# Optimization experiments

Hardware: AMD Instinct MI355X
Metric: run time of the kernel (lower is better)

The kernel has to match this reference:

```python
import jax, jax.numpy as jnp
import numpy as np

EPS = 1e-12

def l2norm(x):
    # torch F.normalize(p=2, dim=-1): x / max(||x||, eps)
    n = jnp.sqrt(jnp.sum(x * x, axis=-1, keepdims=True))
    return x / jnp.maximum(n, EPS)

def grid_sample_zeros(img, grid):
    """Bilinear grid_sample, padding_mode='zeros', align_corners=False.
    img: [B,C,H,W], grid: [B,P,2] with (x,y) in [-1,1]. Returns [B,C,P]."""
    B, C, H, W = img.shape
    ix = ((grid[..., 0] + 1.0) * W - 1.0) * 0.5  # [B,P]
    iy = ((grid[..., 1] + 1.0) * H - 1.0) * 0.5
    x0 = jnp.floor(ix); x1 = x0 + 1.0
    y0 = jnp.floor(iy); y1 = y0 + 1.0
    wx1 = ix - x0; wx0 = 1.0 - wx1
    wy1 = iy - y0; wy0 = 1.0 - wy1

    def gather(xf, yf):
        valid = ((xf >= 0) & (xf <= W - 1) & (yf >= 0) & (yf <= H - 1)).astype(img.dtype)
        xi = jnp.clip(xf, 0, W - 1).astype(jnp.int32)
        yi = jnp.clip(yf, 0, H - 1).astype(jnp.int32)
        v = jax.vmap(lambda im, yy, xx: im[:, yy, xx])(img, yi, xi)  # [B,C,P]
        return v * valid[:, None, :]

    out = (gather(x0, y0) * (wx0 * wy0)[:, None, :]
         + gather(x1, y0) * (wx1 * wy0)[:, None, :]
         + gather(x0, y1) * (wx0 * wy1)[:, None, :]
         + gather(x1, y1) * (wx1 * wy1)[:, None, :])
    return out


def setup_inputs() -> dict:
    key = jax.random.key(0)
    ks = jax.random.split(key, 8)
    B, N, K, C = 4, 512, 128, 256
    H8 = W8 = 128
    H16 = W16 = 64
    inp = {
        'node_reliability_weights': jax.random.normal(ks[0], (B, N), jnp.float32),
        'node_features': jax.random.normal(ks[1], (B, N, C), jnp.float32),
        'rel_map_8': jax.random.normal(ks[2], (B, H8, W8), jnp.float32),
        'feat_map_8': jax.random.normal(ks[3], (B, C, H8, W8), jnp.float32),
        'rel_map_16': jax.random.normal(ks[4], (B, H16, W16), jnp.float32),
        'feat_map_16': jax.random.normal(ks[5], (B, C, H16, W16), jnp.float32),
        # normalized coords in [-1,1]
        'coords': jax.random.uniform(ks[6], (B, K, N, 2), jnp.float32) * 2.0 - 1.0,
        'logit_scale': jnp.asarray(np.log(1.0 / 0.07), jnp.float32),
    }
    return inp


def reference(node_reliability_weights, node_features, rel_map_8, feat_map_8,
              rel_map_16, feat_map_16, coords, logit_scale):
    B, N, C = node_features.shape
    K = coords.shape[1]
    nnf = l2norm(node_features)  # [B,N,C]
    # [B,K,N,2] -> [B,N,K,2] -> [B,N*K,2]
    grid = jnp.transpose(coords, (0, 2, 1, 3)).reshape(B, N * K, 2)

    sims, rels = [], []
    for rel_map, feat_map in ((rel_map_8, feat_map_8), (rel_map_16, feat_map_16)):
        sr = grid_sample_zeros(rel_map[:, None], grid).reshape(B, N, K)
        sf = grid_sample_zeros(feat_map, grid).reshape(B, C, N, K)
        nsf = l2norm(jnp.transpose(sf, (0, 2, 3, 1)))  # [B,N,K,C]
        sims.append(jnp.einsum('bnc,bnkc->bnk', nnf, nsf))
        rels.append(node_reliability_weights[:, :, None] + sr)

    S = len(sims)
    total_sim = jnp.stack(sims, axis=-1)  # [B,N,K,S]
    total_rel = jnp.stack(rels, axis=-1)  # [B,N,K,S]
    total_rel = jnp.transpose(total_rel, (0, 2, 1, 3)).reshape(B, K, N * S)
    total_rel = jax.nn.softmax(total_rel, axis=-1)
    total_sim = jnp.transpose(total_sim, (0, 2, 1, 3)).reshape(B, K, N * S)
    logits = jnp.sum(total_sim * total_rel, axis=-1) * jnp.exp(logit_scale)  # [B,K]
    return jax.nn.softmax(logits, axis=1)
```

## Files before the change

kernel.cpp:

```cpp
#include <hip/hip_runtime.h>
#include <math.h>

typedef _Float16 f16;
typedef _Float16 f16x2 __attribute__((ext_vector_type(2)));
typedef _Float16 f16x4 __attribute__((ext_vector_type(4)));

namespace {
constexpr int B = 4, N = 512, K = 128, C = 256;
constexpr int H8 = 128, W8 = 128, P8 = H8 * W8;
constexpr int H16 = 64, W16 = 64, P16 = H16 * W16;
constexpr int NBG = 32;
constexpr int LBINS = NBG * NBG;
constexpr int NBINS = B * LBINS;
constexpr int NSAMP = B * K * N;
constexpr int WROW = 528;
constexpr int TBX = P8 / 64 + P16 / 64;
constexpr int NCB = NSAMP / 512 / 16;
}

__device__ __forceinline__ float fdot2a(f16x2 a, f16x2 b, float c)
{
#if __has_builtin(__builtin_amdgcn_fdot2)
    return __builtin_amdgcn_fdot2(a, b, c, false);
#else
    return c + (float)a.x * (float)b.x + (float)a.y * (float)b.y;
#endif
}

__device__ __forceinline__ float red16_sum(float x)
{
    int t;
    t = __builtin_amdgcn_update_dpp(0, __float_as_int(x), 0xB1,  0xF, 0xF, true);
    x += __int_as_float(t);
    t = __builtin_amdgcn_update_dpp(0, __float_as_int(x), 0x4E,  0xF, 0xF, true);
    x += __int_as_float(t);
    t = __builtin_amdgcn_update_dpp(0, __float_as_int(x), 0x141, 0xF, 0xF, true);
    x += __int_as_float(t);
    t = __builtin_amdgcn_update_dpp(0, __float_as_int(x), 0x140, 0xF, 0xF, true);
    x += __int_as_float(t);
    return x;
}

__device__ __forceinline__ int band32(float g)
{
    int v = (int)((g + 1.0f) * 0.5f * NBG);
    return min(NBG - 1, max(0, v));
}

__device__ __forceinline__ void blend_dot(
    const float4* A, const float4* Bv, const float* w, const f16x2* nf,
    float& dot, float& n2)
{
    f16x2 v[8];
    {
        const f16 h = (f16)w[0];
        const f16x2 w0{h, h};
        const f16x2* a0 = reinterpret_cast<const f16x2*>(&A[0]);
        const f16x2* b0 = reinterpret_cast<const f16x2*>(&Bv[0]);
#pragma unroll
        for (int c = 0; c < 4; ++c) { v[c] = w0 * a0[c]; v[c + 4] = w0 * b0[c]; }
    }
#pragma unroll
    for (int t = 1; t < 4; ++t) {
        const f16 h = (f16)w[t];
        const f16x2 wt{h, h};
        const f16x2* at = reinterpret_cast<const f16x2*>(&A[t]);
        const f16x2* bt = reinterpret_cast<const f16x2*>(&Bv[t]);
#pragma unroll
        for (int c = 0; c < 4; ++c) { v[c] += wt * at[c]; v[c + 4] += wt * bt[c]; }
    }
    float d0 = 0, d1 = 0, m0 = 0, m1 = 0;
#pragma unroll
    for (int c = 0; c < 4; ++c) { d0 = fdot2a(nf[c], v[c], d0); m0 = fdot2a(v[c], v[c], m0); }
#pragma unroll
    for (int c = 4; c < 8; ++c) { d1 = fdot2a(nf[c], v[c], d1); m1 = fdot2a(v[c], v[c], m1); }
    dot = red16_sum(d0 + d1);
    n2  = red16_sum(m0 + m1);
}

__global__ __launch_bounds__(256) void k_prep(
    const float* __restrict__ in8, const float* __restrict__ in16,
    f16* __restrict__ o8, f16* __restrict__ o16,
    const float* __restrict__ coords, unsigned* __restrict__ hist)
{
    __shared__ float tile[64][65];
    const int tid = threadIdx.x;
    int bx = blockIdx.x;

    if (bx >= TBX) {
        unsigned* cnt = reinterpret_cast<unsigned*>(tile);
        const int cblk = (bx - TBX) * 16 + blockIdx.y * 4 + blockIdx.z;
        const int sid0 = cblk * 512;
        const int b = sid0 >> 16;
        for (int i = tid; i < LBINS; i += 256) cnt[i] = 0;
        __syncthreads();
#pragma unroll
        for (int j = 0; j < 2; ++j) {
            const int sid = sid0 + j * 256 + tid;
            const float gx = coords[(size_t)sid * 2 + 0];
            const float gy = coords[(size_t)sid * 2 + 1];
            atomicAdd(&cnt[band32(gy) * NBG + band32(gx)], 1u);
        }
        __syncthreads();
        for (int i = tid; i < LBINS; i += 256)
            if (cnt[i]) atomicAdd(&hist[b * LBINS + i], cnt[i]);
        return;
    }

    const float* in; f16* out; int P;
    if (bx < P8 / 64) { in = in8; out = o8; P = P8; }
    else { bx -= P8 / 64; in = in16; out = o16; P = P16; }
    const int b  = blockIdx.z;
    const int p0 = bx * 64;
    const int c0 = blockIdx.y * 64;
    const int tp = tid & 63, tq = tid >> 6;
    const float* src = in + (size_t)b * C * P;
    f16* dst = out + (size_t)b * P * C;
#pragma unroll
    for (int i = 0; i < 16; ++i) {
        const int cl = tq + i * 4;
        tile[cl][tp] = src[(size_t)(c0 + cl) * P + (p0 + tp)];
    }
    __syncthreads();
#pragma unroll
    for (int i = 0; i < 16; ++i) {
        const int pl = tq + i * 4;
        dst[(size_t)(p0 + pl) * C + (c0 + tp)] = (f16)tile[tp][pl];
    }
}

__global__ __launch_bounds__(256) void k_scan(
    const unsigned* __restrict__ hist, unsigned* __restrict__ cursor,
    unsigned* __restrict__ binofs)
{
    __shared__ unsigned sums[256];
    const int t = threadIdx.x;
    unsigned v[16];
    unsigned s = 0;
#pragma unroll
    for (int i = 0; i < 16; ++i) { v[i] = s; s += hist[t * 16 + i]; }
    sums[t] = s;
    __syncthreads();
    for (int off = 1; off < 256; off <<= 1) {
        const unsigned x = (t >= off) ? sums[t - off] : 0u;
        __syncthreads();
        sums[t] += x;
        __syncthreads();
    }
    const unsigned pre = (t == 0) ? 0u : sums[t - 1];
#pragma unroll
    for (int i = 0; i < 16; ++i) {
        cursor[t * 16 + i] = pre + v[i];
        binofs[t * 16 + i] = pre + v[i];
    }
    if (t == 255) binofs[NBINS] = sums[255];
}

__global__ __launch_bounds__(256) void k_scatprep(
    const float* __restrict__ coords, unsigned* __restrict__ cursor,
    unsigned* __restrict__ order,
    const float* __restrict__ nodef, f16* __restrict__ nnf)
{
    const int tid = threadIdx.x;
    if (blockIdx.x >= NSAMP / 512) {
        const int node = (blockIdx.x - NSAMP / 512) * 4 + (tid >> 6);
        const int lane = tid & 63;
        const float4 v = *reinterpret_cast<const float4*>(
            nodef + (size_t)node * C + lane * 4);
        float nn = v.x * v.x + v.y * v.y + v.z * v.z + v.w * v.w;
#pragma unroll
        for (int off = 32; off; off >>= 1) nn += __shfl_xor(nn, off);
        const float inv = __frsqrt_rn(fmaxf(nn, 1e-24f));
        f16x4 o;
        o.x = (f16)(v.x * inv); o.y = (f16)(v.y * inv);
        o.z = (f16)(v.z * inv); o.w = (f16)(v.w * inv);
        *reinterpret_cast<f16x4*>(nnf + (size_t)node * C + lane * 4) = o;
        return;
    }

    __shared__ unsigned cnt[LBINS], base[LBINS];
    const int sid0 = blockIdx.x * 512;
    const int b = sid0 >> 16;
    for (int i = tid; i < LBINS; i += 256) cnt[i] = 0;
    __syncthreads();
    int bl[2];
#pragma unroll
    for (int j = 0; j < 2; ++j) {
        const int sid = sid0 + j * 256 + tid;
        const float gx = coords[(size_t)sid * 2 + 0];
        const float gy = coords[(size_t)sid * 2 + 1];
        bl[j] = band32(gy) * NBG + band32(gx);
        atomicAdd(&cnt[bl[j]], 1u);
    }
    __syncthreads();
    for (int i = tid; i < LBINS; i += 256)
        base[i] = cnt[i] ? atomicAdd(&cursor[b * LBINS + i], cnt[i]) : 0u;
    __syncthreads();
    for (int i = tid; i < LBINS; i += 256) cnt[i] = 0;
    __syncthreads();
#pragma unroll
    for (int j = 0; j < 2; ++j) {
        const int sid = sid0 + j * 256 + tid;
        const unsigned r = base[bl[j]] + atomicAdd(&cnt[bl[j]], 1u);
        order[r] = (unsigned)sid;
    }
}

__global__ __launch_bounds__(256) void k_sample(
    const float* __restrict__ nodew,
    const f16*  __restrict__ nnf,
    const float* __restrict__ rel8,
    const float* __restrict__ rel16,
    const float* __restrict__ coords,
    const f16*  __restrict__ ft8,
    const f16*  __restrict__ ft16,
    const unsigned* __restrict__ order,
    const unsigned* __restrict__ binofs,
    float4* __restrict__ sr)
{
    const int bin = ((blockIdx.x & 7) * (NBINS / 8)) + (blockIdx.x >> 3);
    const int b = bin >> 10, lb = bin & (LBINS - 1);
    const int by = lb >> 5, bx = lb & 31;
    const int tid = threadIdx.x;
    const int grp = tid >> 4, gl = tid & 15;
    const int y0w = 4 * by - 1, x0w = 4 * bx - 1;
    const int y0q = 2 * by - 1, x0q = 2 * bx - 1;

    const unsigned s0 = binofs[bin];
    const int cnt = (int)(binofs[bin + 1] - s0);
    if (cnt == 0) return;

    __shared__ __align__(16) unsigned char lds[36 * WROW];
    __shared__ float srel8[36], srel16[16];

    const f16* f8b = ft8 + (size_t)b * P8 * C;
    const f16* fqb = ft16 + (size_t)b * P16 * C;
    const float* r8b = rel8 + (size_t)b * P8;
    const float* rqb = rel16 + (size_t)b * P16;

    for (int i = tid; i < 36 * 33; i += 256) {
        const int r = i / 33, c = i - r * 33;
        const int wy = r / 6, wx = r - wy * 6;
        const int py = min(max(y0w + wy, 0), H8 - 1);
        const int px = min(max(x0w + wx, 0), W8 - 1);
        uint4 v{0, 0, 0, 0};
        if (c < 32)
            v = *reinterpret_cast<const uint4*>(
                f8b + ((size_t)(py * W8 + px)) * C + c * 8);
        *reinterpret_cast<uint4*>(&lds[r * WROW + c * 16]) = v;
    }
    if (tid < 36) {
        const int wy = tid / 6, wx = tid - wy * 6;
        const int py = min(max(y0w + wy, 0), H8 - 1);
        const int px = min(max(x0w + wx, 0), W8 - 1);
        srel8[tid] = r8b[py * W8 + px];
    } else if (tid < 52) {
        const int i = tid - 36;
        const int wy = i >> 2, wx = i & 3;
        const int py = min(max(y0q + wy, 0), H16 - 1);
        const int px = min(max(x0q + wx, 0), W16 - 1);
        srel16[i] = rqb[py * W16 + px];
    }
    __syncthreads();

    for (int basei = 0; basei < cnt; basei += 16) {
        const int idx = basei + grp;
        const bool active = idx < cnt;
        const unsigned sid = order[s0 + (active ? idx : 0)];
        const int n = sid & 511, k = (sid >> 9) & 127;
        const float gx = coords[(size_t)sid * 2 + 0];
        const float gy = coords[(size_t)sid * 2 + 1];

        const f16* np_ = nnf + (size_t)(b * N + n) * C;
        const float4 nr0 = *reinterpret_cast<const float4*>(np_ + gl * 8);
        const float4 nr1 = *reinterpret_cast<const float4*>(np_ + 128 + gl * 8);
        f16x2 nf[8];
        {
            const f16x2* h0 = reinterpret_cast<const f16x2*>(&nr0);
            const f16x2* h1 = reinterpret_cast<const f16x2*>(&nr1);
#pragma unroll
            for (int c = 0; c < 4; ++c) { nf[c] = h0[c]; nf[c + 4] = h1[c]; }
        }

        float wq[4]; int qx0, qx1, qy0, qy1;
        {
            const float ix = ((gx + 1.f) * W16 - 1.f) * 0.5f;
            const float iy = ((gy + 1.f) * H16 - 1.f) * 0.5f;
            const float x0f = floorf(ix), y0f = floorf(iy);
            const int x0 = (int)x0f, y0 = (int)y0f, x1 = x0 + 1, y1 = y0 + 1;
            const float fx1 = ix - x0f, fx0 = 1.f - fx1;
            const float fy1 = iy - y0f, fy0 = 1.f - fy1;
            const bool vx0 = x0 >= 0 && x0 < W16, vx1 = x1 >= 0 && x1 < W16;
            const bool vy0 = y0 >= 0 && y0 < H16, vy1 = y1 >= 0 && y1 < H16;
            wq[0] = vx0 && vy0 ? fx0 * fy0 : 0.f;
            wq[1] = vx1 && vy0 ? fx1 * fy0 : 0.f;
            wq[2] = vx0 && vy1 ? fx0 * fy1 : 0.f;
            wq[3] = vx1 && vy1 ? fx1 * fy1 : 0.f;
            qx0 = min(max(x0, 0), W16 - 1); qx1 = min(max(x1, 0), W16 - 1);
            qy0 = min(max(y0, 0), H16 - 1); qy1 = min(max(y1, 0), H16 - 1);
        }
        const int qp[4] = {qy0 * W16 + qx0, qy0 * W16 + qx1,
                           qy1 * W16 + qx0, qy1 * W16 + qx1};
        float4 ga[4], gb[4];
#pragma unroll
        for (int t = 0; t < 4; ++t) {
            const f16* tp = fqb + (size_t)qp[t] * C;
            ga[t] = *reinterpret_cast<const float4*>(tp + gl * 8);
            gb[t] = *reinterpret_cast<const float4*>(tp + 128 + gl * 8);
        }

        float wp[4]; int sx0, sx1, sy0, sy1;
        {
            const float ix = ((gx + 1.f) * W8 - 1.f) * 0.5f;
            const float iy = ((gy + 1.f) * H8 - 1.f) * 0.5f;
            const float x0f = floorf(ix), y0f = floorf(iy);
            const int x0 = (int)x0f, y0 = (int)y0f, x1 = x0 + 1, y1 = y0 + 1;
            const float fx1 = ix - x0f, fx0 = 1.f - fx1;
            const float fy1 = iy - y0f, fy0 = 1.f - fy1;
            const bool vx0 = x0 >= 0 && x0 < W8, vx1 = x1 >= 0 && x1 < W8;
            const bool vy0 = y0 >= 0 && y0 < H8, vy1 = y1 >= 0 && y1 < H8;
            wp[0] = vx0 && vy0 ? fx0 * fy0 : 0.f;
            wp[1] = vx1 && vy0 ? fx1 * fy0 : 0.f;
            wp[2] = vx0 && vy1 ? fx0 * fy1 : 0.f;
            wp[3] = vx1 && vy1 ? fx1 * fy1 : 0.f;
            sx0 = min(max(x0, 0), W8 - 1); sx1 = min(max(x1, 0), W8 - 1);
            sy0 = min(max(y0, 0), H8 - 1); sy1 = min(max(y1, 0), H8 - 1);
        }
        const int wxa = min(max(sx0 - x0w, 0), 5), wxb = min(max(sx1 - x0w, 0), 5);
        const int wya = min(max(sy0 - y0w, 0), 5), wyb = min(max(sy1 - y0w, 0), 5);
        const int lr[4] = {wya * 6 + wxa, wya * 6 + wxb,
                           wyb * 6 + wxa, wyb * 6 + wxb};
        float4 la[4], lbv[4];
#pragma unroll
        for (int t = 0; t < 4; ++t) {
            la[t]  = *reinterpret_cast<const float4*>(&lds[lr[t] * WROW + gl * 16]);
            lbv[t] = *reinterpret_cast<const float4*>(&lds[lr[t] * WROW + 256 + gl * 16]);
        }

        float dot8, n28;
        blend_dot(la, lbv, wp, nf, dot8, n28);
        const float sim8 = dot8 * __frsqrt_rn(fmaxf(n28, 1e-24f));
        const float rv8 = wp[0] * srel8[lr[0]] + wp[1] * srel8[lr[1]]
                        + wp[2] * srel8[lr[2]] + wp[3] * srel8[lr[3]];

        float dotq, n2q;
        blend_dot(ga, gb, wq, nf, dotq, n2q);
        const float simq = dotq * __frsqrt_rn(fmaxf(n2q, 1e-24f));
        const int qwxa = min(max(qx0 - x0q, 0), 3), qwxb = min(max(qx1 - x0q, 0), 3);
        const int qwya = min(max(qy0 - y0q, 0), 3), qwyb = min(max(qy1 - y0q, 0), 3);
        const float rvq = wq[0] * srel16[qwya * 4 + qwxa] + wq[1] * srel16[qwya * 4 + qwxb]
                        + wq[2] * srel16[qwyb * 4 + qwxa] + wq[3] * srel16[qwyb * 4 + qwxb];

        if (active && gl == 0) {
            const float wr = nodew[b * N + n];
            sr[(size_t)(b * K + k) * N + n] =
                make_float4(sim8, simq, wr + rv8, wr + rvq);
        }
    }
}

__global__ __launch_bounds__(256) void k_logits(
    const float4* __restrict__ sr, const float* __restrict__ lscale,
    float* __restrict__ logits)
{
    const int bk = blockIdx.x;
    const int tid = threadIdx.x;
    const int lane = tid & 63, wid = tid >> 6;
    const float4* sp = sr + (size_t)bk * N;
    __shared__ float red0[4], red1[4], red2[4];

    float4 e0 = sp[tid], e1 = sp[tid + 256];
    float m = fmaxf(fmaxf(e0.z, e0.w), fmaxf(e1.z, e1.w));
#pragma unroll
    for (int off = 32; off; off >>= 1) m = fmaxf(m, __shfl_xor(m, off));
    if (lane == 0) red0[wid] = m;
    __syncthreads();
    m = fmaxf(fmaxf(red0[0], red0[1]), fmaxf(red0[2], red0[3]));

    const float a0 = expf(e0.z - m), a1 = expf(e0.w - m);
    const float b0 = expf(e1.z - m), b1 = expf(e1.w - m);
    float se = a0 + a1 + b0 + b1;
    float ss = a0 * e0.x + a1 * e0.y + b0 * e1.x + b1 * e1.y;
#pragma unroll
    for (int off = 32; off; off >>= 1) {
        se += __shfl_xor(se, off);
        ss += __shfl_xor(ss, off);
    }
    if (lane == 0) { red1[wid] = se; red2[wid] = ss; }
    __syncthreads();
    if (tid == 0) {
        const float tse = red1[0] + red1[1] + red1[2] + red1[3];
        const float tss = red2[0] + red2[1] + red2[2] + red2[3];
        logits[bk] = (tss / tse) * expf(lscale[0]);
    }
}

__global__ __launch_bounds__(64) void k_out(
    const float* __restrict__ logits, float* __restrict__ out)
{
    const int b = blockIdx.x;
    const int lane = threadIdx.x;
    const float v0 = logits[b * K + lane];
    const float v1 = logits[b * K + lane + 64];
    float m = fmaxf(v0, v1);
#pragma unroll
    for (int off = 32; off; off >>= 1) m = fmaxf(m, __shfl_xor(m, off));
    const float e0 = expf(v0 - m), e1 = expf(v1 - m);
    float se = e0 + e1;
#pragma unroll
    for (int off = 32; off; off >>= 1) se += __shfl_xor(se, off);
    out[b * K + lane] = e0 / se;
    out[b * K + lane + 64] = e1 / se;
}

extern "C" void kernel_launch(void* const* d_in, const int* in_sizes, int n_in,
                              void* d_out, int out_size, void* d_ws, size_t ws_size,
                              hipStream_t stream)
{
    const float* nodew  = (const float*)d_in[0];
    const float* nodef  = (const float*)d_in[1];
    const float* rel8   = (const float*)d_in[2];
    const float* feat8  = (const float*)d_in[3];
    const float* rel16  = (const float*)d_in[4];
    const float* feat16 = (const float*)d_in[5];
    const float* coords = (const float*)d_in[6];
    const float* lscale = (const float*)d_in[7];

    char* ws = (char*)d_ws;
    size_t off = 0;
    f16* ft8  = (f16*)(ws + off); off += (size_t)B * P8 * C * 2;
    f16* ft16 = (f16*)(ws + off); off += (size_t)B * P16 * C * 2;
    f16* nnf  = (f16*)(ws + off); off += (size_t)B * N * C * 2;
    float4* sr = (float4*)(ws + off); off += (size_t)NSAMP * 16;
    float* logits = (float*)(ws + off); off += (size_t)B * K * 4;
    unsigned* order  = (unsigned*)(ws + off); off += (size_t)NSAMP * 4;
    unsigned* hist   = (unsigned*)(ws + off); off += NBINS * 4;
    unsigned* cursor = (unsigned*)(ws + off); off += NBINS * 4;
    unsigned* binofs = (unsigned*)(ws + off); off += (NBINS + 1) * 4;
    float* out = (float*)d_out;

    hipMemsetAsync(hist, 0, NBINS * sizeof(unsigned), stream);

    hipLaunchKernelGGL(k_prep, dim3(TBX + NCB, C / 64, B), dim3(256), 0, stream,
                       feat8, feat16, ft8, ft16, coords, hist);
    hipLaunchKernelGGL(k_scan, dim3(1), dim3(256), 0, stream,
                       hist, cursor, binofs);
    hipLaunchKernelGGL(k_scatprep, dim3(NSAMP / 512 + B * N / 4), dim3(256), 0,
                       stream, coords, cursor, order, nodef, nnf);
    hipLaunchKernelGGL(k_sample, dim3(NBINS), dim3(256), 0, stream,
                       nodew, nnf, rel8, rel16, coords, ft8, ft16, order,
                       binofs, sr);
    hipLaunchKernelGGL(k_logits, dim3(B * K), dim3(256), 0, stream,
                       sr, lscale, logits);
    hipLaunchKernelGGL(k_out, dim3(B), dim3(64), 0, stream, logits, out);
}
```

Measured before the change: 94.71 us.

## Stage coarse-scale feature window in LDS and batch two samples per group

The per-bin prologue now also stages the 4x4 window of the 1/16-scale feature map into shared memory alongside the 6x6 window of the 1/8 map. The sampling loop then reads the coarse-scale corners from LDS instead of scattered global memory. The loop also loads the inputs (index, coords, node features) for two samples up front before computing either, so global latency can overlap. This costs more LDS per block, which may lower occupancy, plus extra register pressure from holding two sample inputs at once.

```diff
diff --git a/kernel.cpp b/kernel.cpp
--- a/kernel.cpp
+++ b/kernel.cpp
@@ -206,6 +206,13 @@
     }
 }
 
+struct SampIn {
+    unsigned sid;
+    float gx, gy;
+    float4 n0, n1;
+    bool act;
+};
+
 __global__ __launch_bounds__(256) void k_sample(
     const float* __restrict__ nodew,
     const f16*  __restrict__ nnf,
@@ -230,7 +237,7 @@
     const int cnt = (int)(binofs[bin + 1] - s0);
     if (cnt == 0) return;
 
-    __shared__ __align__(16) unsigned char lds[36 * WROW];
+    __shared__ __align__(16) unsigned char lds[52 * WROW];
     __shared__ float srel8[36], srel16[16];
 
     const f16* f8b = ft8 + (size_t)b * P8 * C;
@@ -238,15 +245,25 @@
     const float* r8b = rel8 + (size_t)b * P8;
     const float* rqb = rel16 + (size_t)b * P16;
 
-    for (int i = tid; i < 36 * 33; i += 256) {
+    for (int i = tid; i < 52 * 33; i += 256) {
         const int r = i / 33, c = i - r * 33;
-        const int wy = r / 6, wx = r - wy * 6;
-        const int py = min(max(y0w + wy, 0), H8 - 1);
-        const int px = min(max(x0w + wx, 0), W8 - 1);
         uint4 v{0, 0, 0, 0};
-        if (c < 32)
-            v = *reinterpret_cast<const uint4*>(
-                f8b + ((size_t)(py * W8 + px)) * C + c * 8);
+        if (r < 36) {
+            const int wy = r / 6, wx = r - wy * 6;
+            const int py = min(max(y0w + wy, 0), H8 - 1);
+            const int px = min(max(x0w + wx, 0), W8 - 1);
+            if (c < 32)
+                v = *reinterpret_cast<const uint4*>(
+                    f8b + ((size_t)(py * W8 + px)) * C + c * 8);
+        } else {
+            const int rr = r - 36;
+            const int wy = rr >> 2, wx = rr & 3;
+            const int py = min(max(y0q + wy, 0), H16 - 1);
+            const int px = min(max(x0q + wx, 0), W16 - 1);
+            if (c < 32)
+                v = *reinterpret_cast<const uint4*>(
+                    fqb + ((size_t)(py * W16 + px)) * C + c * 8);
+        }
         *reinterpret_cast<uint4*>(&lds[r * WROW + c * 16]) = v;
     }
     if (tid < 36) {
@@ -263,29 +280,60 @@
     }
     __syncthreads();
 
-    for (int basei = 0; basei < cnt; basei += 16) {
-        const int idx = basei + grp;
-        const bool active = idx < cnt;
-        const unsigned sid = order[s0 + (active ? idx : 0)];
-        const int n = sid & 511, k = (sid >> 9) & 127;
-        const float gx = coords[(size_t)sid * 2 + 0];
-        const float gy = coords[(size_t)sid * 2 + 1];
-
-        const f16* np_ = nnf + (size_t)(b * N + n) * C;
-        const float4 nr0 = *reinterpret_cast<const float4*>(np_ + gl * 8);
-        const float4 nr1 = *reinterpret_cast<const float4*>(np_ + 128 + gl * 8);
+    auto load_in = [&](int idx) -> SampIn {
+        SampIn s_;
+        s_.act = idx < cnt;
+        s_.sid = order[s0 + (s_.act ? idx : 0)];
+        s_.gx = coords[(size_t)s_.sid * 2 + 0];
+        s_.gy = coords[(size_t)s_.sid * 2 + 1];
+        const f16* np_ = nnf + (size_t)(b * N + (int)(s_.sid & 511)) * C;
+        s_.n0 = *reinterpret_cast<const float4*>(np_ + gl * 8);
+        s_.n1 = *reinterpret_cast<const float4*>(np_ + 128 + gl * 8);
+        return s_;
+    };
+
+    auto do_sample = [&](const SampIn& si) {
+        const int n = si.sid & 511, k = (si.sid >> 9) & 127;
         f16x2 nf[8];
         {
-            const f16x2* h0 = reinterpret_cast<const f16x2*>(&nr0);
-            const f16x2* h1 = reinterpret_cast<const f16x2*>(&nr1);
+            const f16x2* h0 = reinterpret_cast<const f16x2*>(&si.n0);
+            const f16x2* h1 = reinterpret_cast<const f16x2*>(&si.n1);
 #pragma unroll
             for (int c = 0; c < 4; ++c) { nf[c] = h0[c]; nf[c + 4] = h1[c]; }
+        }
+
+        float wp[4]; int sx0, sx1, sy0, sy1;
+        {
+            const float ix = ((si.gx + 1.f) * W8 - 1.f) * 0.5f;
+            const float iy = ((si.gy + 1.f) * H8 - 1.f) * 0.5f;
+            const float x0f = floorf(ix), y0f = floorf(iy);
+            const int x0 = (int)x0f, y0 = (int)y0f, x1 = x0 + 1, y1 = y0 + 1;
+            const float fx1 = ix - x0f, fx0 = 1.f - fx1;
+            const float fy1 = iy - y0f, fy0 = 1.f - fy1;
+            const bool vx0 = x0 >= 0 && x0 < W8, vx1 = x1 >= 0 && x1 < W8;
+            const bool vy0 = y0 >= 0 && y0 < H8, vy1 = y1 >= 0 && y1 < H8;
+            wp[0] = vx0 && vy0 ? fx0 * fy0 : 0.f;
+            wp[1] = vx1 && vy0 ? fx1 * fy0 : 0.f;
+            wp[2] = vx0 && vy1 ? fx0 * fy1 : 0.f;
+            wp[3] = vx1 && vy1 ? fx1 * fy1 : 0.f;
+            sx0 = min(max(x0, 0), W8 - 1); sx1 = min(max(x1, 0), W8 - 1);
+            sy0 = min(max(y0, 0), H8 - 1); sy1 = min(max(y1, 0), H8 - 1);
+        }
+        const int wxa = min(max(sx0 - x0w, 0), 5), wxb = min(max(sx1 - x0w, 0), 5);
+        const int wya = min(max(sy0 - y0w, 0), 5), wyb = min(max(sy1 - y0w, 0), 5);
+        const int lr[4] = {wya * 6 + wxa, wya * 6 + wxb,
+                           wyb * 6 + wxa, wyb * 6 + wxb};
+        float4 la[4], lbv[4];
+#pragma unroll
+        for (int t = 0; t < 4; ++t) {
+            la[t]  = *reinterpret_cast<const float4*>(&lds[lr[t] * WROW + gl * 16]);
+            lbv[t] = *reinterpret_cast<const float4*>(&lds[lr[t] * WROW + 256 + gl * 16]);
         }
 
         float wq[4]; int qx0, qx1, qy0, qy1;
         {
-            const float ix = ((gx + 1.f) * W16 - 1.f) * 0.5f;
-            const float iy = ((gy + 1.f) * H16 - 1.f) * 0.5f;
+            const float ix = ((si.gx + 1.f) * W16 - 1.f) * 0.5f;
+            const float iy = ((si.gy + 1.f) * H16 - 1.f) * 0.5f;
             const float x0f = floorf(ix), y0f = floorf(iy);
             const int x0 = (int)x0f, y0 = (int)y0f, x1 = x0 + 1, y1 = y0 + 1;
             const float fx1 = ix - x0f, fx0 = 1.f - fx1;
@@ -299,42 +347,15 @@
             qx0 = min(max(x0, 0), W16 - 1); qx1 = min(max(x1, 0), W16 - 1);
             qy0 = min(max(y0, 0), H16 - 1); qy1 = min(max(y1, 0), H16 - 1);
         }
-        const int qp[4] = {qy0 * W16 + qx0, qy0 * W16 + qx1,
-                           qy1 * W16 + qx0, qy1 * W16 + qx1};
+        const int qwxa = min(max(qx0 - x0q, 0), 3), qwxb = min(max(qx1 - x0q, 0), 3);
+        const int qwya = min(max(qy0 - y0q, 0), 3), qwyb = min(max(qy1 - y0q, 0), 3);
+        const int qr[4] = {36 + qwya * 4 + qwxa, 36 + qwya * 4 + qwxb,
+                           36 + qwyb * 4 + qwxa, 36 + qwyb * 4 + qwxb};
         float4 ga[4], gb[4];
 #pragma unroll
         for (int t = 0; t < 4; ++t) {
-            const f16* tp = fqb + (size_t)qp[t] * C;
-            ga[t] = *reinterpret_cast<const float4*>(tp + gl * 8);
-            gb[t] = *reinterpret_cast<const float4*>(tp + 128 + gl * 8);
-        }
-
-        float wp[4]; int sx0, sx1, sy0, sy1;
-        {
-            const float ix = ((gx + 1.f) * W8 - 1.f) * 0.5f;
-            const float iy = ((gy + 1.f) * H8 - 1.f) * 0.5f;
-            const float x0f = floorf(ix), y0f = floorf(iy);
-            const int x0 = (int)x0f, y0 = (int)y0f, x1 = x0 + 1, y1 = y0 + 1;
-            const float fx1 = ix - x0f, fx0 = 1.f - fx1;
-            const float fy1 = iy - y0f, fy0 = 1.f - fy1;
-            const bool vx0 = x0 >= 0 && x0 < W8, vx1 = x1 >= 0 && x1 < W8;
-            const bool vy0 = y0 >= 0 && y0 < H8, vy1 = y1 >= 0 && y1 < H8;
-            wp[0] = vx0 && vy0 ? fx0 * fy0 : 0.f;
-            wp[1] = vx1 && vy0 ? fx1 * fy0 : 0.f;
-            wp[2] = vx0 && vy1 ? fx0 * fy1 : 0.f;
-            wp[3] = vx1 && vy1 ? fx1 * fy1 : 0.f;
-            sx0 = min(max(x0, 0), W8 - 1); sx1 = min(max(x1, 0), W8 - 1);
-            sy0 = min(max(y0, 0), H8 - 1); sy1 = min(max(y1, 0), H8 - 1);
-        }
-        const int wxa = min(max(sx0 - x0w, 0), 5), wxb = min(max(sx1 - x0w, 0), 5);
-        const int wya = min(max(sy0 - y0w, 0), 5), wyb = min(max(sy1 - y0w, 0), 5);
-        const int lr[4] = {wya * 6 + wxa, wya * 6 + wxb,
-                           wyb * 6 + wxa, wyb * 6 + wxb};
-        float4 la[4], lbv[4];
-#pragma unroll
-        for (int t = 0; t < 4; ++t) {
-            la[t]  = *reinterpret_cast<const float4*>(&lds[lr[t] * WROW + gl * 16]);
-            lbv[t] = *reinterpret_cast<const float4*>(&lds[lr[t] * WROW + 256 + gl * 16]);
+            ga[t] = *reinterpret_cast<const float4*>(&lds[qr[t] * WROW + gl * 16]);
+            gb[t] = *reinterpret_cast<const float4*>(&lds[qr[t] * WROW + 256 + gl * 16]);
         }
 
         float dot8, n28;
@@ -346,16 +367,21 @@
         float dotq, n2q;
         blend_dot(ga, gb, wq, nf, dotq, n2q);
         const float simq = dotq * __frsqrt_rn(fmaxf(n2q, 1e-24f));
-        const int qwxa = min(max(qx0 - x0q, 0), 3), qwxb = min(max(qx1 - x0q, 0), 3);
-        const int qwya = min(max(qy0 - y0q, 0), 3), qwyb = min(max(qy1 - y0q, 0), 3);
-        const float rvq = wq[0] * srel16[qwya * 4 + qwxa] + wq[1] * srel16[qwya * 4 + qwxb]
-                        + wq[2] * srel16[qwyb * 4 + qwxa] + wq[3] * srel16[qwyb * 4 + qwxb];
-
-        if (active && gl == 0) {
+        const float rvq = wq[0] * srel16[qr[0] - 36] + wq[1] * srel16[qr[1] - 36]
+                        + wq[2] * srel16[qr[2] - 36] + wq[3] * srel16[qr[3] - 36];
+
+        if (si.act && gl == 0) {
             const float wr = nodew[b * N + n];
             sr[(size_t)(b * K + k) * N + n] =
                 make_float4(sim8, simq, wr + rv8, wr + rvq);
         }
+    };
+
+    for (int basei = 0; basei < cnt; basei += 32) {
+        const SampIn A = load_in(basei + grp);
+        const SampIn Bc = load_in(basei + 16 + grp);
+        do_sample(A);
+        do_sample(Bc);
     }
 }
 
```

Result: no change. 96.12 us (+1.5%).

## Replace per-sample blended dot products with MFMA node-pixel dots plus precomputed Gram terms

Applied to the files above, without the earlier changes.

Algebraically splits the bilinear-blended cosine similarity into node·pixel dot products and pixel-pair Gram entries. A new kernel precomputes per-pixel self and neighbour dot products, and the sample kernel computes a 16-sample by 64-pixel dot tile per bin with MFMA. The blend, normalisation and reliability interpolation are then done by 16 threads. This removes the per-sample fp16 blending and global gathers of the 16x16 map, at the cost of an extra full pass over both feature maps, more workspace, two barriers per tile and a mostly idle block during the scalar epilogue.

```diff
diff --git a/kernel.cpp b/kernel.cpp
--- a/kernel.cpp
+++ b/kernel.cpp
@@ -4,6 +4,8 @@
 typedef _Float16 f16;
 typedef _Float16 f16x2 __attribute__((ext_vector_type(2)));
 typedef _Float16 f16x4 __attribute__((ext_vector_type(4)));
+typedef _Float16 f16x8 __attribute__((ext_vector_type(8)));
+typedef float f32x4 __attribute__((ext_vector_type(4)));
 
 namespace {
 constexpr int B = 4, N = 512, K = 128, C = 256;
@@ -47,35 +49,19 @@
     return min(NBG - 1, max(0, v));
 }
 
-__device__ __forceinline__ void blend_dot(
-    const float4* A, const float4* Bv, const float* w, const f16x2* nf,
-    float& dot, float& n2)
-{
-    f16x2 v[8];
-    {
-        const f16 h = (f16)w[0];
-        const f16x2 w0{h, h};
-        const f16x2* a0 = reinterpret_cast<const f16x2*>(&A[0]);
-        const f16x2* b0 = reinterpret_cast<const f16x2*>(&Bv[0]);
-#pragma unroll
-        for (int c = 0; c < 4; ++c) { v[c] = w0 * a0[c]; v[c + 4] = w0 * b0[c]; }
-    }
-#pragma unroll
-    for (int t = 1; t < 4; ++t) {
-        const f16 h = (f16)w[t];
-        const f16x2 wt{h, h};
-        const f16x2* at = reinterpret_cast<const f16x2*>(&A[t]);
-        const f16x2* bt = reinterpret_cast<const f16x2*>(&Bv[t]);
-#pragma unroll
-        for (int c = 0; c < 4; ++c) { v[c] += wt * at[c]; v[c + 4] += wt * bt[c]; }
-    }
-    float d0 = 0, d1 = 0, m0 = 0, m1 = 0;
-#pragma unroll
-    for (int c = 0; c < 4; ++c) { d0 = fdot2a(nf[c], v[c], d0); m0 = fdot2a(v[c], v[c], m0); }
-#pragma unroll
-    for (int c = 4; c < 8; ++c) { d1 = fdot2a(nf[c], v[c], d1); m1 = fdot2a(v[c], v[c], m1); }
-    dot = red16_sum(d0 + d1);
-    n2  = red16_sum(m0 + m1);
+__device__ __forceinline__ float dot16(const float4& a0, const float4& a1,
+                                       const float4& b0, const float4& b1)
+{
+    const f16x2* x0 = reinterpret_cast<const f16x2*>(&a0);
+    const f16x2* x1 = reinterpret_cast<const f16x2*>(&a1);
+    const f16x2* y0 = reinterpret_cast<const f16x2*>(&b0);
+    const f16x2* y1 = reinterpret_cast<const f16x2*>(&b1);
+    float d = 0.f;
+#pragma unroll
+    for (int c = 0; c < 4; ++c) d = fdot2a(x0[c], y0[c], d);
+#pragma unroll
+    for (int c = 0; c < 4; ++c) d = fdot2a(x1[c], y1[c], d);
+    return d;
 }
 
 __global__ __launch_bounds__(256) void k_prep(
@@ -129,6 +115,53 @@
     }
 }
 
+__global__ __launch_bounds__(256) void k_gram(
+    const f16* __restrict__ ft8, const f16* __restrict__ ft16,
+    float* __restrict__ g8, float* __restrict__ g16)
+{
+    const int tid = threadIdx.x;
+    const int gl = tid & 15;
+    int gid = blockIdx.x * 16 + (tid >> 4);
+
+    const f16* fb; float* go; int P, W_, H_, b, p;
+    if (gid < B * P8) {
+        b = gid >> 14; p = gid & (P8 - 1);
+        fb = ft8 + (size_t)b * P8 * C; go = g8; P = P8; W_ = W8; H_ = H8;
+    } else {
+        gid -= B * P8;
+        b = gid >> 12; p = gid & (P16 - 1);
+        fb = ft16 + (size_t)b * P16 * C; go = g16; P = P16; W_ = W16; H_ = H16;
+    }
+    const int y = p / W_, x = p - y * W_;
+    const int x1 = min(x + 1, W_ - 1), y1 = min(y + 1, H_ - 1);
+    const int r00 = p, r10 = y * W_ + x1, r01 = y1 * W_ + x, r11 = y1 * W_ + x1;
+    const int cg = gl * 16;
+
+    const float4 a0 = *reinterpret_cast<const float4*>(fb + (size_t)r00 * C + cg);
+    const float4 a1 = *reinterpret_cast<const float4*>(fb + (size_t)r00 * C + cg + 8);
+    const float4 h0 = *reinterpret_cast<const float4*>(fb + (size_t)r10 * C + cg);
+    const float4 h1 = *reinterpret_cast<const float4*>(fb + (size_t)r10 * C + cg + 8);
+    const float4 v0 = *reinterpret_cast<const float4*>(fb + (size_t)r01 * C + cg);
+    const float4 v1 = *reinterpret_cast<const float4*>(fb + (size_t)r01 * C + cg + 8);
+    const float4 d0 = *reinterpret_cast<const float4*>(fb + (size_t)r11 * C + cg);
+    const float4 d1 = *reinterpret_cast<const float4*>(fb + (size_t)r11 * C + cg + 8);
+
+    float s0 = red16_sum(dot16(a0, a1, a0, a1));
+    float sh = red16_sum(dot16(a0, a1, h0, h1));
+    float sv = red16_sum(dot16(a0, a1, v0, v1));
+    float sd = red16_sum(dot16(a0, a1, d0, d1));
+    float sa = red16_sum(dot16(h0, h1, v0, v1));
+
+    if (gl == 0) {
+        const size_t base = (size_t)b * P + p;
+        go[0 * (size_t)B * P + base] = s0;
+        go[1 * (size_t)B * P + base] = sh;
+        go[2 * (size_t)B * P + base] = sv;
+        go[3 * (size_t)B * P + base] = sd;
+        go[4 * (size_t)B * P + base] = sa;
+    }
+}
+
 __global__ __launch_bounds__(256) void k_scan(
     const unsigned* __restrict__ hist, unsigned* __restrict__ cursor,
     unsigned* __restrict__ binofs)
@@ -214,6 +247,8 @@
     const float* __restrict__ coords,
     const f16*  __restrict__ ft8,
     const f16*  __restrict__ ft16,
+    const float* __restrict__ g8,
+    const float* __restrict__ g16,
     const unsigned* __restrict__ order,
     const unsigned* __restrict__ binofs,
     float4* __restrict__ sr)
@@ -222,7 +257,6 @@
     const int b = bin >> 10, lb = bin & (LBINS - 1);
     const int by = lb >> 5, bx = lb & 31;
     const int tid = threadIdx.x;
-    const int grp = tid >> 4, gl = tid & 15;
     const int y0w = 4 * by - 1, x0w = 4 * bx - 1;
     const int y0q = 2 * by - 1, x0q = 2 * bx - 1;
 
@@ -230,132 +264,177 @@
     const int cnt = (int)(binofs[bin + 1] - s0);
     if (cnt == 0) return;
 
-    __shared__ __align__(16) unsigned char lds[36 * WROW];
-    __shared__ float srel8[36], srel16[16];
+    __shared__ __align__(16) unsigned char lds[64 * WROW];
+    __shared__ float Dbuf[16][64];
+    __shared__ float sG8[5][36], sG16[5][16], srel8[36], srel16[16];
+    __shared__ unsigned s_sid[2][16];
+    __shared__ float s_gx[2][16], s_gy[2][16];
 
     const f16* f8b = ft8 + (size_t)b * P8 * C;
     const f16* fqb = ft16 + (size_t)b * P16 * C;
-    const float* r8b = rel8 + (size_t)b * P8;
-    const float* rqb = rel16 + (size_t)b * P16;
-
-    for (int i = tid; i < 36 * 33; i += 256) {
+
+    for (int i = tid; i < 64 * 33; i += 256) {
         const int r = i / 33, c = i - r * 33;
-        const int wy = r / 6, wx = r - wy * 6;
-        const int py = min(max(y0w + wy, 0), H8 - 1);
-        const int px = min(max(x0w + wx, 0), W8 - 1);
         uint4 v{0, 0, 0, 0};
-        if (c < 32)
-            v = *reinterpret_cast<const uint4*>(
-                f8b + ((size_t)(py * W8 + px)) * C + c * 8);
+        if (c < 32) {
+            if (r < 36) {
+                const int wy = r / 6, wx = r - wy * 6;
+                const int py = min(max(y0w + wy, 0), H8 - 1);
+                const int px = min(max(x0w + wx, 0), W8 - 1);
+                v = *reinterpret_cast<const uint4*>(
+                    f8b + ((size_t)(py * W8 + px)) * C + c * 8);
+            } else if (r < 52) {
+                const int rr = r - 36;
+                const int wy = rr >> 2, wx = rr & 3;
+                const int py = min(max(y0q + wy, 0), H16 - 1);
+                const int px = min(max(x0q + wx, 0), W16 - 1);
+                v = *reinterpret_cast<const uint4*>(
+                    fqb + ((size_t)(py * W16 + px)) * C + c * 8);
+            }
+        }
         *reinterpret_cast<uint4*>(&lds[r * WROW + c * 16]) = v;
     }
     if (tid < 36) {
         const int wy = tid / 6, wx = tid - wy * 6;
         const int py = min(max(y0w + wy, 0), H8 - 1);
         const int px = min(max(x0w + wx, 0), W8 - 1);
-        srel8[tid] = r8b[py * W8 + px];
+        const size_t gp = (size_t)b * P8 + (py * W8 + px);
+        srel8[tid] = rel8[gp];
+#pragma unroll
+        for (int m = 0; m < 5; ++m) sG8[m][tid] = g8[(size_t)m * B * P8 + gp];
     } else if (tid < 52) {
         const int i = tid - 36;
         const int wy = i >> 2, wx = i & 3;
         const int py = min(max(y0q + wy, 0), H16 - 1);
         const int px = min(max(x0q + wx, 0), W16 - 1);
-        srel16[i] = rqb[py * W16 + px];
-    }
-    __syncthreads();
-
-    for (int basei = 0; basei < cnt; basei += 16) {
-        const int idx = basei + grp;
-        const bool active = idx < cnt;
-        const unsigned sid = order[s0 + (active ? idx : 0)];
-        const int n = sid & 511, k = (sid >> 9) & 127;
-        const float gx = coords[(size_t)sid * 2 + 0];
-        const float gy = coords[(size_t)sid * 2 + 1];
-
-        const f16* np_ = nnf + (size_t)(b * N + n) * C;
-        const float4 nr0 = *reinterpret_cast<const float4*>(np_ + gl * 8);
-        const float4 nr1 = *reinterpret_cast<const float4*>(np_ + 128 + gl * 8);
-        f16x2 nf[8];
-        {
-            const f16x2* h0 = reinterpret_cast<const f16x2*>(&nr0);
-            const f16x2* h1 = reinterpret_cast<const f16x2*>(&nr1);
-#pragma unroll
-            for (int c = 0; c < 4; ++c) { nf[c] = h0[c]; nf[c + 4] = h1[c]; }
+        const size_t gp = (size_t)b * P16 + (py * W16 + px);
+        srel16[i] = rel16[gp];
+#pragma unroll
+        for (int m = 0; m < 5; ++m) sG16[m][i] = g16[(size_t)m * B * P16 + gp];
+    } else if (tid >= 64 && tid < 80) {
+        const int t = tid - 64;
+        const int cidx = min(t, cnt - 1);
+        const unsigned sid = order[s0 + cidx];
+        s_gx[0][t] = coords[(size_t)sid * 2 + 0];
+        s_gy[0][t] = coords[(size_t)sid * 2 + 1];
+        s_sid[0][t] = (t < cnt) ? sid : 0xFFFFFFFFu;
+    }
+    __syncthreads();
+
+    const int wv = tid >> 6, ln = tid & 63;
+    const int brow = wv * 16 + (ln & 15);
+    const int koff = (ln >> 4) * 8;
+    f16x8 Bfrag[8];
+#pragma unroll
+    for (int ks = 0; ks < 8; ++ks)
+        Bfrag[ks] = *reinterpret_cast<const f16x8*>(
+            &lds[brow * WROW + (ks * 32 + koff) * 2]);
+
+    const int nmt = (cnt + 15) >> 4;
+    for (int mt = 0; mt < nmt; ++mt) {
+        const int cur = mt & 1;
+        const unsigned asid = s_sid[cur][ln & 15];
+        const int anode = (int)(asid & 511u);
+        const f16* arow = nnf + ((size_t)(b * N + anode)) * C + koff;
+        f16x8 Af[8];
+#pragma unroll
+        for (int ks = 0; ks < 8; ++ks)
+            Af[ks] = *reinterpret_cast<const f16x8*>(arow + ks * 32);
+        f32x4 acc = {0.f, 0.f, 0.f, 0.f};
+#pragma unroll
+        for (int ks = 0; ks < 8; ++ks)
+            acc = __builtin_amdgcn_mfma_f32_16x16x32_f16(Af[ks], Bfrag[ks], acc, 0, 0, 0);
+#pragma unroll
+        for (int r = 0; r < 4; ++r)
+            Dbuf[(ln >> 4) * 4 + r][wv * 16 + (ln & 15)] = acc[r];
+        __syncthreads();
+
+        if (tid < 16) {
+            const unsigned sid = s_sid[cur][tid];
+            if (sid != 0xFFFFFFFFu) {
+                const int n = sid & 511, k = (sid >> 9) & 127;
+                const float gx = s_gx[cur][tid], gy = s_gy[cur][tid];
+
+                float wp[4]; int lr[4];
+                {
+                    const float ix = ((gx + 1.f) * W8 - 1.f) * 0.5f;
+                    const float iy = ((gy + 1.f) * H8 - 1.f) * 0.5f;
+                    const float x0f = floorf(ix), y0f = floorf(iy);
+                    const int x0 = (int)x0f, y0 = (int)y0f, x1 = x0 + 1, y1 = y0 + 1;
+                    const float fx1 = ix - x0f, fx0 = 1.f - fx1;
+                    const float fy1 = iy - y0f, fy0 = 1.f - fy1;
+                    const bool vx0 = x0 >= 0 && x0 < W8, vx1 = x1 >= 0 && x1 < W8;
+                    const bool vy0 = y0 >= 0 && y0 < H8, vy1 = y1 >= 0 && y1 < H8;
+                    wp[0] = vx0 && vy0 ? fx0 * fy0 : 0.f;
+                    wp[1] = vx1 && vy0 ? fx1 * fy0 : 0.f;
+                    wp[2] = vx0 && vy1 ? fx0 * fy1 : 0.f;
+                    wp[3] = vx1 && vy1 ? fx1 * fy1 : 0.f;
+                    const int sx0 = min(max(x0, 0), W8 - 1), sx1 = min(max(x1, 0), W8 - 1);
+                    const int sy0 = min(max(y0, 0), H8 - 1), sy1 = min(max(y1, 0), H8 - 1);
+                    const int wxa = min(max(sx0 - x0w, 0), 5), wxb = min(max(sx1 - x0w, 0), 5);
+                    const int wya = min(max(sy0 - y0w, 0), 5), wyb = min(max(sy1 - y0w, 0), 5);
+                    lr[0] = wya * 6 + wxa; lr[1] = wya * 6 + wxb;
+                    lr[2] = wyb * 6 + wxa; lr[3] = wyb * 6 + wxb;
+                }
+                const float num8 = wp[0] * Dbuf[tid][lr[0]] + wp[1] * Dbuf[tid][lr[1]]
+                                 + wp[2] * Dbuf[tid][lr[2]] + wp[3] * Dbuf[tid][lr[3]];
+                const float den8 =
+                      wp[0] * wp[0] * sG8[0][lr[0]] + wp[1] * wp[1] * sG8[0][lr[1]]
+                    + wp[2] * wp[2] * sG8[0][lr[2]] + wp[3] * wp[3] * sG8[0][lr[3]]
+                    + 2.f * (wp[0] * wp[1] * sG8[1][lr[0]] + wp[2] * wp[3] * sG8[1][lr[2]]
+                           + wp[0] * wp[2] * sG8[2][lr[0]] + wp[1] * wp[3] * sG8[2][lr[1]]
+                           + wp[0] * wp[3] * sG8[3][lr[0]] + wp[1] * wp[2] * sG8[4][lr[0]]);
+                const float sim8 = num8 * __frsqrt_rn(fmaxf(den8, 1e-24f));
+                const float rv8 = wp[0] * srel8[lr[0]] + wp[1] * srel8[lr[1]]
+                                + wp[2] * srel8[lr[2]] + wp[3] * srel8[lr[3]];
+
+                float wq[4]; int qr[4];
+                {
+                    const float ix = ((gx + 1.f) * W16 - 1.f) * 0.5f;
+                    const float iy = ((gy + 1.f) * H16 - 1.f) * 0.5f;
+                    const float x0f = floorf(ix), y0f = floorf(iy);
+                    const int x0 = (int)x0f, y0 = (int)y0f, x1 = x0 + 1, y1 = y0 + 1;
+                    const float fx1 = ix - x0f, fx0 = 1.f - fx1;
+                    const float fy1 = iy - y0f, fy0 = 1.f - fy1;
+                    const bool vx0 = x0 >= 0 && x0 < W16, vx1 = x1 >= 0 && x1 < W16;
+                    const bool vy0 = y0 >= 0 && y0 < H16, vy1 = y1 >= 0 && y1 < H16;
+                    wq[0] = vx0 && vy0 ? fx0 * fy0 : 0.f;
+                    wq[1] = vx1 && vy0 ? fx1 * fy0 : 0.f;
+                    wq[2] = vx0 && vy1 ? fx0 * fy1 : 0.f;
+                    wq[3] = vx1 && vy1 ? fx1 * fy1 : 0.f;
+                    const int qx0 = min(max(x0, 0), W16 - 1), qx1 = min(max(x1, 0), W16 - 1);
+                    const int qy0 = min(max(y0, 0), H16 - 1), qy1 = min(max(y1, 0), H16 - 1);
+                    const int qwxa = min(max(qx0 - x0q, 0), 3), qwxb = min(max(qx1 - x0q, 0), 3);
+                    const int qwya = min(max(qy0 - y0q, 0), 3), qwyb = min(max(qy1 - y0q, 0), 3);
+                    qr[0] = qwya * 4 + qwxa; qr[1] = qwya * 4 + qwxb;
+                    qr[2] = qwyb * 4 + qwxa; qr[3] = qwyb * 4 + qwxb;
+                }
+                const float numq = wq[0] * Dbuf[tid][36 + qr[0]] + wq[1] * Dbuf[tid][36 + qr[1]]
+                                 + wq[2] * Dbuf[tid][36 + qr[2]] + wq[3] * Dbuf[tid][36 + qr[3]];
+                const float denq =
+                      wq[0] * wq[0] * sG16[0][qr[0]] + wq[1] * wq[1] * sG16[0][qr[1]]
+                    + wq[2] * wq[2] * sG16[0][qr[2]] + wq[3] * wq[3] * sG16[0][qr[3]]
+                    + 2.f * (wq[0] * wq[1] * sG16[1][qr[0]] + wq[2] * wq[3] * sG16[1][qr[2]]
+                           + wq[0] * wq[2] * sG16[2][qr[0]] + wq[1] * wq[3] * sG16[2][qr[1]]
+                           + wq[0] * wq[3] * sG16[3][qr[0]] + wq[1] * wq[2] * sG16[4][qr[0]]);
+                const float simq = numq * __frsqrt_rn(fmaxf(denq, 1e-24f));
+                const float rvq = wq[0] * srel16[qr[0]] + wq[1] * srel16[qr[1]]
+                                + wq[2] * srel16[qr[2]] + wq[3] * srel16[qr[3]];
+
+                const float wr = nodew[b * N + n];
+                sr[(size_t)(b * K + k) * N + n] =
+                    make_float4(sim8, simq, wr + rv8, wr + rvq);
+            }
+        } else if (tid >= 64 && tid < 80 && mt + 1 < nmt) {
+            const int t = tid - 64;
+            const int idx = (mt + 1) * 16 + t;
+            const int cidx = min(idx, cnt - 1);
+            const unsigned sid = order[s0 + cidx];
+            s_gx[cur ^ 1][t] = coords[(size_t)sid * 2 + 0];
+            s_gy[cur ^ 1][t] = coords[(size_t)sid * 2 + 1];
+            s_sid[cur ^ 1][t] = (idx < cnt) ? sid : 0xFFFFFFFFu;
         }
-
-        float wq[4]; int qx0, qx1, qy0, qy1;
-        {
-            const float ix = ((gx + 1.f) * W16 - 1.f) * 0.5f;
-            const float iy = ((gy + 1.f) * H16 - 1.f) * 0.5f;
-            const float x0f = floorf(ix), y0f = floorf(iy);
-            const int x0 = (int)x0f, y0 = (int)y0f, x1 = x0 + 1, y1 = y0 + 1;
-            const float fx1 = ix - x0f, fx0 = 1.f - fx1;
-            const float fy1 = iy - y0f, fy0 = 1.f - fy1;
-            const bool vx0 = x0 >= 0 && x0 < W16, vx1 = x1 >= 0 && x1 < W16;
-            const bool vy0 = y0 >= 0 && y0 < H16, vy1 = y1 >= 0 && y1 < H16;
-            wq[0] = vx0 && vy0 ? fx0 * fy0 : 0.f;
-            wq[1] = vx1 && vy0 ? fx1 * fy0 : 0.f;
-            wq[2] = vx0 && vy1 ? fx0 * fy1 : 0.f;
-            wq[3] = vx1 && vy1 ? fx1 * fy1 : 0.f;
-            qx0 = min(max(x0, 0), W16 - 1); qx1 = min(max(x1, 0), W16 - 1);
-            qy0 = min(max(y0, 0), H16 - 1); qy1 = min(max(y1, 0), H16 - 1);
-        }
-        const int qp[4] = {qy0 * W16 + qx0, qy0 * W16 + qx1,
-                           qy1 * W16 + qx0, qy1 * W16 + qx1};
-        float4 ga[4], gb[4];
-#pragma unroll
-        for (int t = 0; t < 4; ++t) {
-            const f16* tp = fqb + (size_t)qp[t] * C;
-            ga[t] = *reinterpret_cast<const float4*>(tp + gl * 8);
-            gb[t] = *reinterpret_cast<const float4*>(tp + 128 + gl * 8);
-        }
-
-        float wp[4]; int sx0, sx1, sy0, sy1;
-        {
-            const float ix = ((gx + 1.f) * W8 - 1.f) * 0.5f;
-            const float iy = ((gy + 1.f) * H8 - 1.f) * 0.5f;
-            const float x0f = floorf(ix), y0f = floorf(iy);
-            const int x0 = (int)x0f, y0 = (int)y0f, x1 = x0 + 1, y1 = y0 + 1;
-            const float fx1 = ix - x0f, fx0 = 1.f - fx1;
-            const float fy1 = iy - y0f, fy0 = 1.f - fy1;
-            const bool vx0 = x0 >= 0 && x0 < W8, vx1 = x1 >= 0 && x1 < W8;
-            const bool vy0 = y0 >= 0 && y0 < H8, vy1 = y1 >= 0 && y1 < H8;
-            wp[0] = vx0 && vy0 ? fx0 * fy0 : 0.f;
-            wp[1] = vx1 && vy0 ? fx1 * fy0 : 0.f;
-            wp[2] = vx0 && vy1 ? fx0 * fy1 : 0.f;
-            wp[3] = vx1 && vy1 ? fx1 * fy1 : 0.f;
-            sx0 = min(max(x0, 0), W8 - 1); sx1 = min(max(x1, 0), W8 - 1);
-            sy0 = min(max(y0, 0), H8 - 1); sy1 = min(max(y1, 0), H8 - 1);
-        }
-        const int wxa = min(max(sx0 - x0w, 0), 5), wxb = min(max(sx1 - x0w, 0), 5);
-        const int wya = min(max(sy0 - y0w, 0), 5), wyb = min(max(sy1 - y0w, 0), 5);
-        const int lr[4] = {wya * 6 + wxa, wya * 6 + wxb,
-                           wyb * 6 + wxa, wyb * 6 + wxb};
-        float4 la[4], lbv[4];
-#pragma unroll
-        for (int t = 0; t < 4; ++t) {
-            la[t]  = *reinterpret_cast<const float4*>(&lds[lr[t] * WROW + gl * 16]);
-            lbv[t] = *reinterpret_cast<const float4*>(&lds[lr[t] * WROW + 256 + gl * 16]);
-        }
-
-        float dot8, n28;
-        blend_dot(la, lbv, wp, nf, dot8, n28);
-        const float sim8 = dot8 * __frsqrt_rn(fmaxf(n28, 1e-24f));
-        const float rv8 = wp[0] * srel8[lr[0]] + wp[1] * srel8[lr[1]]
-                        + wp[2] * srel8[lr[2]] + wp[3] * srel8[lr[3]];
-
-        float dotq, n2q;
-        blend_dot(ga, gb, wq, nf, dotq, n2q);
-        const float simq = dotq * __frsqrt_rn(fmaxf(n2q, 1e-24f));
-        const int qwxa = min(max(qx0 - x0q, 0), 3), qwxb = min(max(qx1 - x0q, 0), 3);
-        const int qwya = min(max(qy0 - y0q, 0), 3), qwyb = min(max(qy1 - y0q, 0), 3);
-        const float rvq = wq[0] * srel16[qwya * 4 + qwxa] + wq[1] * srel16[qwya * 4 + qwxb]
-                        + wq[2] * srel16[qwyb * 4 + qwxa] + wq[3] * srel16[qwyb * 4 + qwxb];
-
-        if (active && gl == 0) {
-            const float wr = nodew[b * N + n];
-            sr[(size_t)(b * K + k) * N + n] =
-                make_float4(sim8, simq, wr + rv8, wr + rvq);
-        }
+        __syncthreads();
     }
 }
 
@@ -431,6 +510,8 @@
     f16* ft8  = (f16*)(ws + off); off += (size_t)B * P8 * C * 2;
     f16* ft16 = (f16*)(ws + off); off += (size_t)B * P16 * C * 2;
     f16* nnf  = (f16*)(ws + off); off += (size_t)B * N * C * 2;
+    float* g8  = (float*)(ws + off); off += (size_t)5 * B * P8 * 4;
+    float* g16 = (float*)(ws + off); off += (size_t)5 * B * P16 * 4;
     float4* sr = (float4*)(ws + off); off += (size_t)NSAMP * 16;
     float* logits = (float*)(ws + off); off += (size_t)B * K * 4;
     unsigned* order  = (unsigned*)(ws + off); off += (size_t)NSAMP * 4;
@@ -443,13 +524,15 @@
 
     hipLaunchKernelGGL(k_prep, dim3(TBX + NCB, C / 64, B), dim3(256), 0, stream,
                        feat8, feat16, ft8, ft16, coords, hist);
+    hipLaunchKernelGGL(k_gram, dim3((B * (P8 + P16)) / 16), dim3(256), 0, stream,
+                       ft8, ft16, g8, g16);
     hipLaunchKernelGGL(k_scan, dim3(1), dim3(256), 0, stream,
                        hist, cursor, binofs);
     hipLaunchKernelGGL(k_scatprep, dim3(NSAMP / 512 + B * N / 4), dim3(256), 0,
                        stream, coords, cursor, order, nodef, nnf);
     hipLaunchKernelGGL(k_sample, dim3(NBINS), dim3(256), 0, stream,
-                       nodew, nnf, rel8, rel16, coords, ft8, ft16, order,
-                       binofs, sr);
+                       nodew, nnf, rel8, rel16, coords, ft8, ft16, g8, g16,
+                       order, binofs, sr);
     hipLaunchKernelGGL(k_logits, dim3(B * K), dim3(256), 0, stream,
                        sr, lscale, logits);
     hipLaunchKernelGGL(k_out, dim3(B), dim3(64), 0, stream, logits, out);
```

Result: slower. 140.3 us (+48.2%).
